# Kernel tuning notes

Hardware: AMD Instinct MI355X
Metric: run time of the kernel (lower is better)

Reference implementation:

```python
import jax, jax.numpy as jnp
import numpy as np

EPS = 1e-5


def reference(hidden_states, mu_x, W_x1, W_x2, x_bias, W_r, W_k, W_v, W_g,
              A_w, B_w, b_w, bonus, gn_weight, gn_bias, W_o):
    B, T, D = hidden_states.shape
    Hh = bonus.shape[0]
    x = hidden_states
    # token shift: delta = shifted(x) - x, shifted pads one zero row at t=0
    shifted = jnp.pad(x, ((0, 0), (1, 0), (0, 0)))[:, :T]
    delta = shifted - x
    # x_proj: LerpLinear(D -> 5*lr) -> tanh -> einsum with second weight viewed [D,5,lr]
    lr = W_x1.shape[0] // 5
    z = jnp.tanh((x + delta * mu_x) @ W_x1.T).reshape(B, T, 5, lr)
    mus = jnp.einsum('blnr,dnr->blnd', z, W_x2.reshape(D, 5, lr)) + x_bias  # [B,T,5,D]
    r_mu, w_mu, k_mu, v_mu, g_mu = (mus[:, :, i] for i in range(5))
    # DDLerpLinear projections: linear(x + delta * mu)
    r = (x + delta * r_mu) @ W_r.T                                 # [B,T,KD]
    w = jnp.tanh((x + delta * w_mu) @ A_w.T) @ B_w.T + b_w          # LoRA w/ tanh
    k = (x + delta * k_mu) @ W_k.T
    v = (x + delta * v_mu) @ W_v.T                                 # [B,T,VD]
    g = (x + delta * g_mu) @ W_g.T
    K = W_r.shape[0] // Hh
    V = W_v.shape[0] // Hh
    r = r.reshape(B, T, Hh, K)
    k = k.reshape(B, T, Hh, K)
    w = -jnp.exp(w.reshape(B, T, Hh, K))  # log-decay, in (-inf, 0)
    v = v.reshape(B, T, Hh, V)
    u = bonus                              # [Hh, K]

    def step(S, inp):
        q_t, k_t, v_t, w_t = inp           # [B,Hh,K],[B,Hh,K],[B,Hh,V],[B,Hh,K]
        kv = k_t[..., :, None] * v_t[..., None, :]                  # [B,Hh,K,V]
        o_t = jnp.einsum('bhk,bhkv->bhv', q_t, S + u[None, :, :, None] * kv)
        S = jnp.exp(w_t)[..., None] * S + kv
        return S, o_t

    S0 = jnp.zeros((B, Hh, K, V), dtype=x.dtype)
    xs = (jnp.swapaxes(r, 0, 1), jnp.swapaxes(k, 0, 1),
          jnp.swapaxes(v, 0, 1), jnp.swapaxes(w, 0, 1))
    _, o = jax.lax.scan(step, S0, xs)       # o: [T,B,Hh,V]
    o = jnp.swapaxes(o, 0, 1)               # [B,T,Hh,V]
    # GroupNorm(num_heads, value_dim): normalize each head's V channels per token
    mean = o.mean(-1, keepdims=True)
    var = o.var(-1, keepdims=True)
    o = (o - mean) / jnp.sqrt(var + EPS)
    o = o.reshape(B, T, Hh * V) * gn_weight + gn_bias
    o = o * jax.nn.silu(g)                  # swish gate
    return o @ W_o.T


def setup_inputs() -> dict:
    key = jax.random.key(0)
    ks = jax.random.split(key, 16)
    B, T, D = 8, 2048, 1024
    Hh, KD, VD, LR, GLR = 4, 512, 1024, 32, 64
    s = 0.02
    w = lambda k, shape: jax.random.normal(k, shape, jnp.float32) * s
    return {
        'hidden_states': jax.random.normal(ks[0], (B, T, D), jnp.float32),
        'mu_x': w(ks[1], (D,)),
        'W_x1': w(ks[2], (5 * LR, D)),
        'W_x2': w(ks[3], (D, 5 * LR)),
        'x_bias': jnp.zeros((5, D), jnp.float32),
        'W_r': w(ks[4], (KD, D)),
        'W_k': w(ks[5], (KD, D)),
        'W_v': w(ks[6], (VD, D)),
        'W_g': w(ks[7], (VD, D)),
        'A_w': w(ks[8], (GLR, D)),
        'B_w': w(ks[9], (KD, GLR)),
        'b_w': jnp.zeros((KD,), jnp.float32),
        'bonus': w(ks[10], (Hh, KD // Hh)),
        'gn_weight': jnp.ones((VD,), jnp.float32),
        'gn_bias': jnp.zeros((VD,), jnp.float32),
        'W_o': w(ks[11], (D, VD)),
    }
```

## Files before the change

kernel.cpp:

```cpp
#include <hip/hip_runtime.h>
#include <hip/hip_bf16.h>
#include <hip/hip_fp16.h>
#include <cstdint>


typedef _Float16 half8 __attribute__((ext_vector_type(8)));
typedef float f32x4 __attribute__((ext_vector_type(4)));

#define CL 256
#define NP (CL / 2)
#define NC 8

__device__ __forceinline__ float hbits2f(unsigned short us) {
    __half h; *reinterpret_cast<unsigned short*>(&h) = us; return __half2float(h);
}
__device__ __forceinline__ unsigned short f2h(float f) {
    __half h = __float2half(f);
    return *reinterpret_cast<unsigned short*>(&h);
}
__device__ __forceinline__ float2 up2(unsigned int u) {
    return make_float2(hbits2f((unsigned short)(u & 0xFFFF)),
                       hbits2f((unsigned short)(u >> 16)));
}
__device__ __forceinline__ void gload_lds16(const void* g, void* l) {
    __builtin_amdgcn_global_load_lds(
        (const __attribute__((address_space(1))) unsigned*)g,
        (__attribute__((address_space(3))) unsigned*)l, 16, 0, 0);
}

__global__ __launch_bounds__(256) void cast_all(
    const float* __restrict__ p0, const float* __restrict__ p1,
    const float* __restrict__ p2, const float* __restrict__ p3,
    const float* __restrict__ p4, const float* __restrict__ p5,
    const float* __restrict__ p6, const float* __restrict__ p7,
    const float* __restrict__ p8, __half* __restrict__ dst)
{
    const int v = blockIdx.x * 256 + threadIdx.x;
    const float* s; int off;
    if      (v < 40960)  { s = p0; off = v; }
    else if (v < 81920)  { s = p1; off = v - 40960; }
    else if (v < 212992) { s = p2; off = v - 81920; }
    else if (v < 344064) { s = p3; off = v - 212992; }
    else if (v < 606208) { s = p4; off = v - 344064; }
    else if (v < 868352) { s = p5; off = v - 606208; }
    else if (v < 884736) { s = p6; off = v - 868352; }
    else if (v < 892928) { s = p7; off = v - 884736; }
    else                 { s = p8; off = v - 892928; }
    const float4 f = *(const float4*)(s + (size_t)off * 4);
    ushort4 u;
    u.x = f2h(f.x); u.y = f2h(f.y); u.z = f2h(f.z); u.w = f2h(f.w);
    *(ushort4*)(dst + (size_t)v * 4) = u;
}

__global__ __launch_bounds__(256) void cast_x(const float* __restrict__ x,
                                              __half* __restrict__ xh)
{
    const size_t v = (size_t)blockIdx.x * 256 + threadIdx.x;
    const float4 f = *(const float4*)(x + v * 4);
    ushort4 u;
    u.x = f2h(f.x); u.y = f2h(f.y); u.z = f2h(f.z); u.w = f2h(f.w);
    *(ushort4*)(xh + v * 4) = u;
}

__global__ void k_xw_h(const float* __restrict__ X, const float* __restrict__ mu,
                       __half* __restrict__ XW, int M, int T)
{
    const size_t i4 = (size_t)blockIdx.x * blockDim.x + threadIdx.x;
    if (i4 >= (size_t)M * 256) return;
    const size_t idx = i4 * 4;
    const int m = (int)(idx >> 10);
    const int d = (int)(idx & 1023);
    const int t = m & (T - 1);
    const float4 xv = *(const float4*)(X + idx);
    const float4 m4 = *(const float4*)(mu + d);
    float4 xp = make_float4(0.f, 0.f, 0.f, 0.f);
    if (t > 0) xp = *(const float4*)(X + idx - 1024);
    ushort4 o;
    o.x = f2h(xv.x + (xp.x - xv.x) * m4.x);
    o.y = f2h(xv.y + (xp.y - xv.y) * m4.y);
    o.z = f2h(xv.z + (xp.z - xv.z) * m4.z);
    o.w = f2h(xv.w + (xp.w - xv.w) * m4.w);
    *(ushort4*)(XW + idx) = o;
}

__global__ __launch_bounds__(256) void gemm16(
    const __half* __restrict__ A, int lda,
    const __half* __restrict__ B, int ldb,
    void* __restrict__ Cv, int ldc,
    int M, int N, int K,
    const float* __restrict__ bias, int epi,
    const __half* __restrict__ X, int T)
{
    __shared__ __align__(16) _Float16 As[128 * 32];
    __shared__ __align__(16) _Float16 Bs[128 * 32];

    const int tid = threadIdx.x;

    const int nwg = gridDim.x * gridDim.y;
    int p = blockIdx.y * gridDim.x + blockIdx.x;
    if (!(nwg & 7)) p = (p & 7) * (nwg >> 3) + (p >> 3);
    const int bx = p % gridDim.x, by = p / gridDim.x;

    const int m0 = by * 128;
    const int n0 = bx * 128;
    const int wave = tid >> 6, lane = tid & 63;
    const int wm = wave >> 1, wn = wave & 1;
    const int lr = lane & 15, lk = lane >> 4;

    const int srow = tid >> 2;
    const int scol = (tid & 3) * 8;
    const int arow0 = m0 + srow, arow1 = m0 + 64 + srow;
    int brow0 = n0 + srow;      if (brow0 >= N) brow0 = N - 1;
    int brow1 = n0 + 64 + srow; if (brow1 >= N) brow1 = N - 1;
    char* dA = (char*)As + tid * 16;
    char* dB = (char*)Bs + tid * 16;

    f32x4 acc[4][4] = {};

    for (int k0 = 0; k0 < K; k0 += 32) {
        const __half* gA0 = A + (size_t)arow0 * lda + k0 + scol;
        const __half* gA1 = A + (size_t)arow1 * lda + k0 + scol;
        const __half* gB0 = B + (size_t)brow0 * ldb + k0 + scol;
        const __half* gB1 = B + (size_t)brow1 * ldb + k0 + scol;
        __syncthreads();
        gload_lds16(gA0, dA);
        gload_lds16(gA1, dA + 4096);
        gload_lds16(gB0, dB);
        gload_lds16(gB1, dB + 4096);
        __syncthreads();

        half8 af[4], bf[4];
#pragma unroll
        for (int f = 0; f < 4; f++) {
            af[f] = *(const half8*)&As[(wm * 64 + f * 16 + lr) * 32 + lk * 8];
            bf[f] = *(const half8*)&Bs[(wn * 64 + f * 16 + lr) * 32 + lk * 8];
        }
#pragma unroll
        for (int fm = 0; fm < 4; fm++)
#pragma unroll
            for (int fn = 0; fn < 4; fn++)
                acc[fm][fn] = __builtin_amdgcn_mfma_f32_16x16x32_f16(
                    af[fm], bf[fn], acc[fm][fn], 0, 0, 0);
    }

#pragma unroll
    for (int fm = 0; fm < 4; fm++) {
#pragma unroll
        for (int fn = 0; fn < 4; fn++) {
            const int gm0 = m0 + wm * 64 + fm * 16 + lk * 4;
            const int gn = n0 + wn * 64 + fn * 16 + lr;
            if (gn >= N) continue;
            float xprev = 0.f;
            if (epi == 2 && (gm0 & (T - 1)))
                xprev = __half2float(X[(size_t)(gm0 - 1) * 1024 + gn]);
#pragma unroll
            for (int j = 0; j < 4; j++) {
                const int gm = gm0 + j;
                float a = acc[fm][fn][j];
                if (epi == 1) {
                    a = tanhf(a);
                    ((__half*)Cv)[(size_t)gm * ldc + gn] = __float2half(a);
                } else if (epi == 2) {
                    a += bias[gn];
                    const float xv = __half2float(X[(size_t)gm * 1024 + gn]);
                    ((__half*)Cv)[(size_t)gm * ldc + gn] =
                        __float2half(xv + (xprev - xv) * a);
                    xprev = xv;
                } else if (epi == 3) {
                    a += bias[gn];
                    ((__half*)Cv)[(size_t)gm * ldc + gn] = __float2half(a);
                } else if (epi == 4) {
                    ((float*)Cv)[(size_t)gm * ldc + gn] = a;
                } else {
                    ((__half*)Cv)[(size_t)gm * ldc + gn] = __float2half(a);
                }
            }
        }
    }
}

__global__ __launch_bounds__(256) void k_prep(
    const __half* __restrict__ R, const __half* __restrict__ Kk,
    const __half* __restrict__ W, const float* __restrict__ bonus,
    unsigned* __restrict__ Eu, float* __restrict__ RU, int T)
{
    const int tok = blockIdx.x;
    const int b = tok >> 11, t = tok & 2047;
    const int h = threadIdx.x >> 6, lane = threadIdx.x & 63;
    const size_t base = (size_t)tok * 512 + h * 128 + 2 * lane;
    const unsigned rr = *(const unsigned*)(R + base);
    const unsigned kk = *(const unsigned*)(Kk + base);
    const unsigned ww = *(const unsigned*)(W + base);
    const float2 rf = up2(rr), kf = up2(kk), wf = up2(ww);
    const float d0 = __expf(-__expf(wf.x));
    const float d1 = __expf(-__expf(wf.y));
    const float2 uf = *(const float2*)(bonus + h * 128 + 2 * lane);
    float ru = rf.x * uf.x * kf.x + rf.y * uf.y * kf.y;
#pragma unroll
    for (int off = 1; off < 64; off <<= 1) ru += __shfl_xor(ru, off);
    const int bh = b * 4 + h;
    unsigned* ep = Eu + (size_t)(bh * T + t) * 192;
    uint2 rkw;
    rkw.x = (rr & 0xFFFFu) | (kk << 16);
    rkw.y = (rr >> 16) | (kk & 0xFFFF0000u);
    *(uint2*)(ep + 2 * lane) = rkw;
    ep[128 + lane] = (unsigned)f2h(d0) | ((unsigned)f2h(d1) << 16);
    if (lane == 0) RU[(size_t)bh * T + t] = ru;
}

__global__ __launch_bounds__(128) void a_gen(
    const unsigned* __restrict__ Eu, __half* __restrict__ Ab,
    float* __restrict__ Abuf, int T)
{
    const int p = blockIdx.x;
    const int l = (p & 7) * 28 + (p >> 3);
    const int bh = l / 7, ci = l - bh * 7;
    const int c = ci + 1;
    const int k = threadIdx.x;
    const int t0 = c * CL;
    const unsigned* ep = Eu + (size_t)(bh * T + t0) * 192;
    __half* ap = Ab + ((size_t)bh * T + t0) * 128 + k;
    const int sel = (k & 1) * 16;
    float D = 1.f;
#pragma unroll 4
    for (int t = 0; t < CL; ++t) {
        const unsigned* e = ep + (size_t)t * 192;
        const unsigned rk = e[k];
        const unsigned dw = e[128 + (k >> 1)];
        const float r = hbits2f((unsigned short)(rk & 0xFFFF));
        const float d = hbits2f((unsigned short)((dw >> sel) & 0xFFFF));
        ap[(size_t)t * 128] = __float2half(r * D);
        D *= d;
    }
    if (c < NC - 1) Abuf[(size_t)(c * 32 + bh) * 128 + k] = D;
}

__global__ __launch_bounds__(256) void rwkv_scan(
    const uint4* __restrict__ E, const __half* __restrict__ V,
    const float* __restrict__ RU, __half* __restrict__ Cout,
    __half* __restrict__ O, int T)
{
    __shared__ uint4 sE[4][96];
    __shared__ uint4 sV[4][16];
    __shared__ float sRU[4][2];

    const int p = blockIdx.x;
    const int l = (p & 7) * 128 + (p >> 3);
    const int bh = l >> 5, c = (l >> 2) & 7, vq = l & 3;
    const int b = bh >> 2, h = bh & 3;
    const int tid = threadIdx.x;
    const int w = tid >> 6, lane = tid & 63;
    const int kg = tid & 15, vg = tid >> 4;
    const int t0 = c * CL;

    const uint4* Eg = E + (size_t)(bh * T + t0) * 48;
    const uint4* Vgp = (const uint4*)(V + ((size_t)b * T + t0) * 1024 + h * 256 + vq * 64);
    const float* RUp = RU + (size_t)bh * T + t0;
    __half* Op = O + ((size_t)b * T + t0) * 1024 + h * 256 + vq * 64 + vg * 4;

    float S[32];
#pragma unroll
    for (int j = 0; j < 32; j++) S[j] = 0.f;

    const int i0 = (kg * 2) ^ ((kg * 2) >> 3);
    const int i1 = (kg * 2 + 1) ^ ((kg * 2 + 1) >> 3);

#define ISSUE(BE, BV, BR, PP)                                                 \
    if (w < 2 && (PP) < NP) {                                                 \
        const int tt = (PP) * 2 + w;                                          \
        if (lane < 48)      BE = Eg[(size_t)tt * 48 + lane];                  \
        else if (lane < 56) BV = Vgp[(size_t)tt * 128 + (lane - 48)];         \
        if (lane == 56)     BR = RUp[tt];                                     \
    }

#define STAGE(BE, BV, BR, SLOT)                                               \
    if (w < 2) {                                                              \
        if (lane < 32)      sE[SLOT][w * 48 + (lane ^ (lane >> 3))] = BE;     \
        else if (lane < 48) sE[SLOT][w * 48 + lane] = BE;                     \
        else if (lane < 56) sV[SLOT][w * 8 + (lane - 48)] = BV;               \
        if (lane == 56)     sRU[SLOT][w] = BR;                                \
    }

#define BAR() do {                                                            \
        asm volatile("s_waitcnt lgkmcnt(0)" ::: "memory");                    \
        __builtin_amdgcn_s_barrier();                                         \
        __builtin_amdgcn_sched_barrier(0);                                    \
    } while (0)

#define COMPUTE(SLOT, SUB, TT)                                                \
    {                                                                         \
        const uint4 rka = sE[SLOT][(SUB) * 48 + i0];                          \
        const uint4 rkb = sE[SLOT][(SUB) * 48 + i1];                          \
        const uint4 dq  = sE[SLOT][(SUB) * 48 + 32 + kg];                     \
        const uint2 vw  = *(const uint2*)((const unsigned*)&sV[SLOT][(SUB) * 8] + vg * 2); \
        const unsigned rw_[8] = {rka.x, rka.y, rka.z, rka.w,                  \
                                 rkb.x, rkb.y, rkb.z, rkb.w};                 \
        const unsigned dw_[4] = {dq.x, dq.y, dq.z, dq.w};                     \
        float r_[8], k_[8], d_[8], vv_[4];                                    \
        _Pragma("unroll") for (int j = 0; j < 8; j++) {                       \
            const float2 rk = up2(rw_[j]); r_[j] = rk.x; k_[j] = rk.y;        \
        }                                                                     \
        _Pragma("unroll") for (int j = 0; j < 4; j++) {                       \
            const float2 dd = up2(dw_[j]); d_[2 * j] = dd.x; d_[2 * j + 1] = dd.y; \
        }                                                                     \
        { const float2 va = up2(vw.x), vb = up2(vw.y);                        \
          vv_[0] = va.x; vv_[1] = va.y; vv_[2] = vb.x; vv_[3] = vb.y; }       \
        float osum[4] = {0.f, 0.f, 0.f, 0.f};                                 \
        _Pragma("unroll") for (int kk = 0; kk < 8; kk++) {                    \
            _Pragma("unroll") for (int vi = 0; vi < 4; vi++) {                \
                osum[vi] = fmaf(r_[kk], S[kk * 4 + vi], osum[vi]);            \
                S[kk * 4 + vi] = fmaf(d_[kk], S[kk * 4 + vi], k_[kk] * vv_[vi]); \
            }                                                                 \
        }                                                                     \
        _Pragma("unroll") for (int vi = 0; vi < 4; vi++) {                    \
            osum[vi] += __shfl_xor(osum[vi], 1);                              \
            osum[vi] += __shfl_xor(osum[vi], 2);                              \
            osum[vi] += __shfl_xor(osum[vi], 4);                              \
            osum[vi] += __shfl_xor(osum[vi], 8);                              \
        }                                                                     \
        if (kg == 0) {                                                        \
            const float ru_ = sRU[SLOT][SUB];                                 \
            ushort4 ou;                                                       \
            ou.x = f2h(osum[0] + ru_ * vv_[0]);                               \
            ou.y = f2h(osum[1] + ru_ * vv_[1]);                               \
            ou.z = f2h(osum[2] + ru_ * vv_[2]);                               \
            ou.w = f2h(osum[3] + ru_ * vv_[3]);                               \
            *(ushort4*)(Op + (size_t)(TT) * 1024) = ou;                       \
        }                                                                     \
    }

#define COMPUTE2(SLOT, PP)  COMPUTE(SLOT, 0, (PP) * 2) COMPUTE(SLOT, 1, (PP) * 2 + 1)

    uint4 e0 = {}, e1 = {}, e2 = {}, e3 = {};
    uint4 v0 = {}, v1 = {}, v2 = {}, v3 = {};
    float r0 = 0.f, r1 = 0.f, r2 = 0.f, r3 = 0.f;

    ISSUE(e0, v0, r0, 0)
    ISSUE(e1, v1, r1, 1)
    ISSUE(e2, v2, r2, 2)
    ISSUE(e3, v3, r3, 3)
    STAGE(e0, v0, r0, 0)
    BAR();

    for (int ps = 0; ps < NP; ps += 4) {
        STAGE(e1, v1, r1, 1)
        ISSUE(e0, v0, r0, ps + 4)
        COMPUTE2(0, ps)
        BAR();
        STAGE(e2, v2, r2, 2)
        ISSUE(e1, v1, r1, ps + 5)
        COMPUTE2(1, ps + 1)
        BAR();
        STAGE(e3, v3, r3, 3)
        ISSUE(e2, v2, r2, ps + 6)
        COMPUTE2(2, ps + 2)
        BAR();
        if (ps + 4 < NP) STAGE(e0, v0, r0, 0)
        ISSUE(e3, v3, r3, ps + 7)
        COMPUTE2(3, ps + 3)
        BAR();
    }

    if (c < NC - 1) {
        __half* Cw = Cout + ((size_t)c * 32 + bh) * 32768 +
                     (size_t)(vq * 64 + vg * 4) * 128 + kg * 8;
#pragma unroll
        for (int vi = 0; vi < 4; vi++) {
            unsigned su[4];
#pragma unroll
            for (int j = 0; j < 4; j++)
                su[j] = (unsigned)f2h(S[(2 * j) * 4 + vi]) |
                        ((unsigned)f2h(S[(2 * j + 1) * 4 + vi]) << 16);
            uint4 s4; s4.x = su[0]; s4.y = su[1]; s4.z = su[2]; s4.w = su[3];
            *(uint4*)(Cw + (size_t)vi * 128) = s4;
        }
    }
#undef ISSUE
#undef STAGE
#undef BAR
#undef COMPUTE
#undef COMPUTE2
}

__global__ __launch_bounds__(256) void rwkv_comb(
    __half* __restrict__ C, const float* __restrict__ A)
{
    const int gid = blockIdx.x * 256 + threadIdx.x;
    const int bh = gid >> 15;
    const int elem = gid & 32767;
    const int k = elem & 127;
    float s = hbits2f(*(const unsigned short*)(C + (size_t)bh * 32768 + elem));
#pragma unroll
    for (int c = 1; c < NC - 1; ++c) {
        const float a = A[(size_t)(c * 32 + bh) * 128 + k];
        __half* cp = C + ((size_t)c * 32 + bh) * 32768 + elem;
        s = a * s + hbits2f(*(const unsigned short*)cp);
        *(unsigned short*)cp = f2h(s);
    }
}

__global__ __launch_bounds__(256) void corr_gemm(
    const __half* __restrict__ Abig, const __half* __restrict__ Cbuf,
    __half* __restrict__ O, int T)
{
    __shared__ __align__(16) _Float16 As[128 * 32];
    __shared__ __align__(16) _Float16 Bs[128 * 32];

    const int tid = threadIdx.x;
    const int p = blockIdx.x;
    const int l = (p & 7) * 112 + (p >> 3);
    const int bhc = l >> 2, mt = (l >> 1) & 1, nt = l & 1;
    const int bh = bhc / 7, ci = bhc - bh * 7;
    const int b = bh >> 2, h = bh & 3;
    const int t0 = (ci + 1) * CL + mt * 128;

    const __half* Ag = Abig + ((size_t)bh * T + t0) * 128;
    const __half* Bg = Cbuf + ((size_t)ci * 32 + bh) * 32768 + (size_t)nt * 128 * 128;
    __half* Og = O + ((size_t)b * T + t0) * 1024 + h * 256 + nt * 128;

    const int wave = tid >> 6, lane = tid & 63;
    const int wm = wave >> 1, wn = wave & 1;
    const int lr = lane & 15, lk = lane >> 4;
    const int srow = tid >> 2;
    const int scol = (tid & 3) * 8;
    char* dA = (char*)As + tid * 16;
    char* dB = (char*)Bs + tid * 16;

    f32x4 acc[4][4] = {};

    for (int k0 = 0; k0 < 128; k0 += 32) {
        const __half* gA0 = Ag + (size_t)srow * 128 + k0 + scol;
        const __half* gA1 = Ag + (size_t)(64 + srow) * 128 + k0 + scol;
        const __half* gB0 = Bg + (size_t)srow * 128 + k0 + scol;
        const __half* gB1 = Bg + (size_t)(64 + srow) * 128 + k0 + scol;
        __syncthreads();
        gload_lds16(gA0, dA);
        gload_lds16(gA1, dA + 4096);
        gload_lds16(gB0, dB);
        gload_lds16(gB1, dB + 4096);
        __syncthreads();

        half8 af[4], bf[4];
#pragma unroll
        for (int f = 0; f < 4; f++) {
            af[f] = *(const half8*)&As[(wm * 64 + f * 16 + lr) * 32 + lk * 8];
            bf[f] = *(const half8*)&Bs[(wn * 64 + f * 16 + lr) * 32 + lk * 8];
        }
#pragma unroll
        for (int fm = 0; fm < 4; fm++)
#pragma unroll
            for (int fn = 0; fn < 4; fn++)
                acc[fm][fn] = __builtin_amdgcn_mfma_f32_16x16x32_f16(
                    af[fm], bf[fn], acc[fm][fn], 0, 0, 0);
    }

#pragma unroll
    for (int fm = 0; fm < 4; fm++) {
#pragma unroll
        for (int fn = 0; fn < 4; fn++) {
#pragma unroll
            for (int j = 0; j < 4; j++) {
                const int row = wm * 64 + fm * 16 + lk * 4 + j;
                const int col = wn * 64 + fn * 16 + lr;
                __half* op = Og + (size_t)row * 1024 + col;
                *op = __float2half(__half2float(*op) + acc[fm][fn][j]);
            }
        }
    }
}

__global__ __launch_bounds__(256) void gn_gate(
    const __half* __restrict__ Obuf, const __half* __restrict__ G,
    const float* __restrict__ gnw, const float* __restrict__ gnb,
    __half* __restrict__ Y)
{
    const int token = blockIdx.x;
    const int wave = threadIdx.x >> 6, lane = threadIdx.x & 63;
    const size_t base = (size_t)token * 1024 + wave * 256 + lane * 4;
    const ushort4 xu = *(const ushort4*)(Obuf + base);
    const float x0 = hbits2f(xu.x), x1 = hbits2f(xu.y),
                x2 = hbits2f(xu.z), x3 = hbits2f(xu.w);
    float sum = x0 + x1 + x2 + x3;
    float ssq = x0 * x0 + x1 * x1 + x2 * x2 + x3 * x3;
#pragma unroll
    for (int off = 32; off >= 1; off >>= 1) {
        sum += __shfl_xor(sum, off);
        ssq += __shfl_xor(ssq, off);
    }
    const float mean = sum * (1.f / 256.f);
    const float var = ssq * (1.f / 256.f) - mean * mean;
    const float rstd = rsqrtf(var + 1e-5f);
    const int c0 = wave * 256 + lane * 4;
    const float4 w4 = *(const float4*)(gnw + c0);
    const float4 b4 = *(const float4*)(gnb + c0);
    const ushort4 gu = *(const ushort4*)(G + base);
    const float g0 = hbits2f(gu.x), g1 = hbits2f(gu.y),
                g2 = hbits2f(gu.z), g3 = hbits2f(gu.w);
    ushort4 y;
    y.x = f2h(((x0 - mean) * rstd * w4.x + b4.x) * (g0 / (1.f + __expf(-g0))));
    y.y = f2h(((x1 - mean) * rstd * w4.y + b4.y) * (g1 / (1.f + __expf(-g1))));
    y.z = f2h(((x2 - mean) * rstd * w4.z + b4.z) * (g2 / (1.f + __expf(-g2))));
    y.w = f2h(((x3 - mean) * rstd * w4.w + b4.w) * (g3 / (1.f + __expf(-g3))));
    *(ushort4*)(Y + base) = y;
}

extern "C" void kernel_launch(void* const* d_in, const int* in_sizes, int n_in,
                              void* d_out, int out_size, void* d_ws, size_t ws_size,
                              hipStream_t stream)
{
    (void)in_sizes; (void)n_in; (void)out_size; (void)ws_size;
    const float* x      = (const float*)d_in[0];
    const float* mu_x   = (const float*)d_in[1];
    const float* W_x1   = (const float*)d_in[2];
    const float* W_x2   = (const float*)d_in[3];
    const float* x_bias = (const float*)d_in[4];
    const float* W_r    = (const float*)d_in[5];
    const float* W_k    = (const float*)d_in[6];
    const float* W_v    = (const float*)d_in[7];
    const float* W_g    = (const float*)d_in[8];
    const float* A_w    = (const float*)d_in[9];
    const float* B_w    = (const float*)d_in[10];
    const float* b_w    = (const float*)d_in[11];
    const float* bonus  = (const float*)d_in[12];
    const float* gnw    = (const float*)d_in[13];
    const float* gnb    = (const float*)d_in[14];
    const float* W_o    = (const float*)d_in[15];

    const int B = 8, T = 2048, M = B * T;

    __half* xwh  = (__half*)d_out;
    __half* inbh = xwh + (size_t)M * 1024;
    __half* xh   = xwh;
    __half* Abig = (__half*)((char*)d_out + (size_t)48 * 1024 * 1024);

    __half* z   = (__half*)d_ws;
    __half* w1  = z   + (size_t)M * 160;
    __half* rs  = w1  + (size_t)M * 64;
    __half* ks  = rs  + (size_t)M * 512;
    __half* wsm = ks  + (size_t)M * 512;
    __half* vs  = wsm + (size_t)M * 512;
    __half* gs  = vs  + (size_t)M * 1024;
    float*  ru  = (float*)(gs + (size_t)M * 1024);
    __half* wgt = (__half*)(ru + (size_t)32 * T);
    __half* oh  = rs;
    __half* yb  = wsm;
    __half* Cbuf = wsm;
    float*  Abuf = (float*)z;

    __half* W_x1h = wgt;
    __half* W_x2h = W_x1h + 163840;
    __half* W_rh  = W_x2h + 163840;
    __half* W_kh  = W_rh + 524288;
    __half* W_vh  = W_kh + 524288;
    __half* W_gh  = W_vh + 1048576;
    __half* A_wh  = W_gh + 1048576;
    __half* B_wh  = A_wh + 65536;
    __half* W_oh  = B_wh + 32768;

    const dim3 blk(256);
    cast_all<<<dim3(4512), blk, 0, stream>>>(W_x1, W_x2, W_r, W_k, W_v, W_g,
                                             A_w, B_w, W_o, wgt);

    k_xw_h<<<(M * 256 + 255) / 256, blk, 0, stream>>>(x, mu_x, xwh, M, T);

    auto ggrid = [&](int N) { return dim3((N + 127) / 128, M / 128); };

    gemm16<<<ggrid(160), blk, 0, stream>>>(xwh, 1024, W_x1h, 1024, z, 160,
                                           M, 160, 1024, nullptr, 1, nullptr, T);

    cast_x<<<dim3(16384), blk, 0, stream>>>(x, xh);

    for (int n = 0; n < 5; ++n) {
        gemm16<<<ggrid(1024), blk, 0, stream>>>(z + n * 32, 160, W_x2h + n * 32, 160,
                                                inbh, 1024, M, 1024, 32,
                                                x_bias + n * 1024, 2, xh, T);
        if (n == 1) {
            gemm16<<<ggrid(64), blk, 0, stream>>>(inbh, 1024, A_wh, 1024, w1, 64,
                                                  M, 64, 1024, nullptr, 1, nullptr, T);
            gemm16<<<ggrid(512), blk, 0, stream>>>(w1, 64, B_wh, 64, wsm, 512,
                                                   M, 512, 64, b_w, 3, nullptr, T);
        } else {
            __half* Cp = (n == 0) ? rs : (n == 2) ? ks : (n == 3) ? vs : gs;
            const __half* Wp = (n == 0) ? W_rh : (n == 2) ? W_kh : (n == 3) ? W_vh : W_gh;
            const int N = (n == 0 || n == 2) ? 512 : 1024;
            gemm16<<<ggrid(N), blk, 0, stream>>>(inbh, 1024, Wp, 1024, Cp, N,
                                                 M, N, 1024, nullptr, 0, nullptr, T);
        }
    }

    k_prep<<<dim3(M), blk, 0, stream>>>(rs, ks, wsm, bonus,
                                        (unsigned*)d_out, ru, T);

    a_gen<<<dim3(224), dim3(128), 0, stream>>>((const unsigned*)d_out, Abig,
                                               Abuf, T);

    rwkv_scan<<<dim3(1024), blk, 0, stream>>>(
        (const uint4*)d_out, vs, ru, Cbuf, oh, T);
    rwkv_comb<<<dim3(4096), blk, 0, stream>>>(Cbuf, Abuf);
    corr_gemm<<<dim3(896), blk, 0, stream>>>(Abig, Cbuf, oh, T);

    gn_gate<<<dim3(M), blk, 0, stream>>>(oh, gs, gnw, gnb, yb);

    gemm16<<<ggrid(1024), blk, 0, stream>>>(yb, 1024, W_oh, 1024, d_out, 1024,
                                            M, 1024, 1024, nullptr, 4, nullptr, T);
}
```

Measured before the change: 1.071 ms.

## Widen rwkv_scan per-thread V tile to 8 columns and halve block count

Each scan block now covers 128 V columns per head instead of 64, so every thread keeps 64 state values (8 K × 8 V) and the grid shrinks from 1024 to 512 blocks. The aim is to load and unpack the r/k/decay rows and run the shuffle reductions once per 8 V columns rather than per 4, cutting the amount of E data loaded per unit of work. The RU load moves to wave 2, V staging now uses all remaining lanes of waves 0-1, and outputs and chunk states are written in wider stores. The cost is higher register pressure from the doubled state array and fewer blocks to hide latency.

```diff
diff --git a/kernel.cpp b/kernel.cpp
--- a/kernel.cpp
+++ b/kernel.cpp
@@ -241,12 +241,12 @@
     __half* __restrict__ O, int T)
 {
     __shared__ uint4 sE[4][96];
-    __shared__ uint4 sV[4][16];
+    __shared__ uint4 sV[4][32];
     __shared__ float sRU[4][2];
 
     const int p = blockIdx.x;
-    const int l = (p & 7) * 128 + (p >> 3);
-    const int bh = l >> 5, c = (l >> 2) & 7, vq = l & 3;
+    const int l = (p & 7) * 64 + (p >> 3);
+    const int bh = l >> 4, c = (l >> 1) & 7, vq = l & 1;
     const int b = bh >> 2, h = bh & 3;
     const int tid = threadIdx.x;
     const int w = tid >> 6, lane = tid & 63;
@@ -254,31 +254,35 @@
     const int t0 = c * CL;
 
     const uint4* Eg = E + (size_t)(bh * T + t0) * 48;
-    const uint4* Vgp = (const uint4*)(V + ((size_t)b * T + t0) * 1024 + h * 256 + vq * 64);
+    const uint4* Vgp = (const uint4*)(V + ((size_t)b * T + t0) * 1024 + h * 256 + vq * 128);
     const float* RUp = RU + (size_t)bh * T + t0;
-    __half* Op = O + ((size_t)b * T + t0) * 1024 + h * 256 + vq * 64 + vg * 4;
-
-    float S[32];
-#pragma unroll
-    for (int j = 0; j < 32; j++) S[j] = 0.f;
+    __half* Op = O + ((size_t)b * T + t0) * 1024 + h * 256 + vq * 128 + vg * 8;
+
+    float S[64];
+#pragma unroll
+    for (int j = 0; j < 64; j++) S[j] = 0.f;
 
     const int i0 = (kg * 2) ^ ((kg * 2) >> 3);
     const int i1 = (kg * 2 + 1) ^ ((kg * 2 + 1) >> 3);
 
 #define ISSUE(BE, BV, BR, PP)                                                 \
-    if (w < 2 && (PP) < NP) {                                                 \
-        const int tt = (PP) * 2 + w;                                          \
-        if (lane < 48)      BE = Eg[(size_t)tt * 48 + lane];                  \
-        else if (lane < 56) BV = Vgp[(size_t)tt * 128 + (lane - 48)];         \
-        if (lane == 56)     BR = RUp[tt];                                     \
+    if ((PP) < NP) {                                                          \
+        if (w < 2) {                                                          \
+            const int tt = (PP) * 2 + w;                                      \
+            if (lane < 48) BE = Eg[(size_t)tt * 48 + lane];                   \
+            else           BV = Vgp[(size_t)tt * 128 + (lane - 48)];          \
+        } else if (w == 2 && lane < 2) {                                      \
+            BR = RUp[(PP) * 2 + lane];                                        \
+        }                                                                     \
     }
 
 #define STAGE(BE, BV, BR, SLOT)                                               \
     if (w < 2) {                                                              \
         if (lane < 32)      sE[SLOT][w * 48 + (lane ^ (lane >> 3))] = BE;     \
         else if (lane < 48) sE[SLOT][w * 48 + lane] = BE;                     \
-        else if (lane < 56) sV[SLOT][w * 8 + (lane - 48)] = BV;               \
-        if (lane == 56)     sRU[SLOT][w] = BR;                                \
+        else                sV[SLOT][w * 16 + (lane - 48)] = BV;              \
+    } else if (w == 2 && lane < 2) {                                          \
+        sRU[SLOT][lane] = BR;                                                 \
     }
 
 #define BAR() do {                                                            \
@@ -292,27 +296,27 @@
         const uint4 rka = sE[SLOT][(SUB) * 48 + i0];                          \
         const uint4 rkb = sE[SLOT][(SUB) * 48 + i1];                          \
         const uint4 dq  = sE[SLOT][(SUB) * 48 + 32 + kg];                     \
-        const uint2 vw  = *(const uint2*)((const unsigned*)&sV[SLOT][(SUB) * 8] + vg * 2); \
+        const uint4 vq4 = sV[SLOT][(SUB) * 16 + vg];                          \
         const unsigned rw_[8] = {rka.x, rka.y, rka.z, rka.w,                  \
                                  rkb.x, rkb.y, rkb.z, rkb.w};                 \
         const unsigned dw_[4] = {dq.x, dq.y, dq.z, dq.w};                     \
-        float r_[8], k_[8], d_[8], vv_[4];                                    \
+        const unsigned vw_[4] = {vq4.x, vq4.y, vq4.z, vq4.w};                 \
+        float r_[8], k_[8], d_[8], vv_[8];                                    \
         _Pragma("unroll") for (int j = 0; j < 8; j++) {                       \
             const float2 rk = up2(rw_[j]); r_[j] = rk.x; k_[j] = rk.y;        \
         }                                                                     \
         _Pragma("unroll") for (int j = 0; j < 4; j++) {                       \
             const float2 dd = up2(dw_[j]); d_[2 * j] = dd.x; d_[2 * j + 1] = dd.y; \
+            const float2 vv = up2(vw_[j]); vv_[2 * j] = vv.x; vv_[2 * j + 1] = vv.y; \
         }                                                                     \
-        { const float2 va = up2(vw.x), vb = up2(vw.y);                        \
-          vv_[0] = va.x; vv_[1] = va.y; vv_[2] = vb.x; vv_[3] = vb.y; }       \
-        float osum[4] = {0.f, 0.f, 0.f, 0.f};                                 \
+        float osum[8] = {0.f, 0.f, 0.f, 0.f, 0.f, 0.f, 0.f, 0.f};             \
         _Pragma("unroll") for (int kk = 0; kk < 8; kk++) {                    \
-            _Pragma("unroll") for (int vi = 0; vi < 4; vi++) {                \
-                osum[vi] = fmaf(r_[kk], S[kk * 4 + vi], osum[vi]);            \
-                S[kk * 4 + vi] = fmaf(d_[kk], S[kk * 4 + vi], k_[kk] * vv_[vi]); \
+            _Pragma("unroll") for (int vi = 0; vi < 8; vi++) {                \
+                osum[vi] = fmaf(r_[kk], S[kk * 8 + vi], osum[vi]);            \
+                S[kk * 8 + vi] = fmaf(d_[kk], S[kk * 8 + vi], k_[kk] * vv_[vi]); \
             }                                                                 \
         }                                                                     \
-        _Pragma("unroll") for (int vi = 0; vi < 4; vi++) {                    \
+        _Pragma("unroll") for (int vi = 0; vi < 8; vi++) {                    \
             osum[vi] += __shfl_xor(osum[vi], 1);                              \
             osum[vi] += __shfl_xor(osum[vi], 2);                              \
             osum[vi] += __shfl_xor(osum[vi], 4);                              \
@@ -320,12 +324,12 @@
         }                                                                     \
         if (kg == 0) {                                                        \
             const float ru_ = sRU[SLOT][SUB];                                 \
-            ushort4 ou;                                                       \
-            ou.x = f2h(osum[0] + ru_ * vv_[0]);                               \
-            ou.y = f2h(osum[1] + ru_ * vv_[1]);                               \
-            ou.z = f2h(osum[2] + ru_ * vv_[2]);                               \
-            ou.w = f2h(osum[3] + ru_ * vv_[3]);                               \
-            *(ushort4*)(Op + (size_t)(TT) * 1024) = ou;                       \
+            unsigned ou[4];                                                   \
+            _Pragma("unroll") for (int j = 0; j < 4; j++)                     \
+                ou[j] = (unsigned)f2h(osum[2 * j] + ru_ * vv_[2 * j]) |       \
+                        ((unsigned)f2h(osum[2 * j + 1] + ru_ * vv_[2 * j + 1]) << 16); \
+            uint4 o4; o4.x = ou[0]; o4.y = ou[1]; o4.z = ou[2]; o4.w = ou[3]; \
+            *(uint4*)(Op + (size_t)(TT) * 1024) = o4;                         \
         }                                                                     \
     }
 
@@ -362,17 +366,17 @@
     }
 
     if (c < NC - 1) {
-        __half* Cw = Cout + ((size_t)c * 32 + bh) * 32768 +
-                     (size_t)(vq * 64 + vg * 4) * 128 + kg * 8;
-#pragma unroll
-        for (int vi = 0; vi < 4; vi++) {
+#pragma unroll
+        for (int vi = 0; vi < 8; vi++) {
+            __half* Cw = Cout + ((size_t)c * 32 + bh) * 32768 +
+                         (size_t)(vq * 128 + vg * 8 + vi) * 128 + kg * 8;
             unsigned su[4];
 #pragma unroll
             for (int j = 0; j < 4; j++)
-                su[j] = (unsigned)f2h(S[(2 * j) * 4 + vi]) |
-                        ((unsigned)f2h(S[(2 * j + 1) * 4 + vi]) << 16);
+                su[j] = (unsigned)f2h(S[(2 * j) * 8 + vi]) |
+                        ((unsigned)f2h(S[(2 * j + 1) * 8 + vi]) << 16);
             uint4 s4; s4.x = su[0]; s4.y = su[1]; s4.z = su[2]; s4.w = su[3];
-            *(uint4*)(Cw + (size_t)vi * 128) = s4;
+            *(uint4*)Cw = s4;
         }
     }
 #undef ISSUE
@@ -594,7 +598,7 @@
     a_gen<<<dim3(224), dim3(128), 0, stream>>>((const unsigned*)d_out, Abig,
                                                Abuf, T);
 
-    rwkv_scan<<<dim3(1024), blk, 0, stream>>>(
+    rwkv_scan<<<dim3(512), blk, 0, stream>>>(
         (const uint4*)d_out, vs, ru, Cbuf, oh, T);
     rwkv_comb<<<dim3(4096), blk, 0, stream>>>(Cbuf, Abuf);
     corr_gemm<<<dim3(896), blk, 0, stream>>>(Abig, Cbuf, oh, T);
```

After: 1.081 ms. Within noise of the previous version (+0.9%).
